# Kernel tuning notes

Measured on AMD Instinct MI355X. Metric: run time of the kernel, lower is better.

The kernel has to match this reference:

```python
import jax, jax.numpy as jnp
import numpy as np

DIM, NH, NKV, HD = 4096, 32, 8, 128
N_REP = NH // NKV
START_POS = 32767  # decode position; cache holds positions [0, START_POS)


def _rope(x, cos, sin):
    # x: (B, L, H, D); cos/sin: (L, D/2). Complex multiply on (even, odd) pairs.
    b, l, h, d = x.shape
    xr = x.reshape(b, l, h, d // 2, 2)
    x0, x1 = xr[..., 0], xr[..., 1]
    c = cos[None, :, None, :]
    s = sin[None, :, None, :]
    o0 = x0 * c - x1 * s
    o1 = x0 * s + x1 * c
    return jnp.stack([o0, o1], axis=-1).reshape(b, l, h, d)


def setup_inputs() -> dict:
    key = jax.random.key(0)
    ks = jax.random.split(key, 8)
    x = jax.random.normal(ks[0], (1, 1, DIM), jnp.float32)
    # real RoPE angles for the current position
    inv_freq = 1.0 / (10000.0 ** (np.arange(0, HD, 2, dtype=np.float32) / HD))
    ang = jnp.asarray((START_POS * inv_freq)[None, :], jnp.float32)  # (1, 64)
    freqs_cos = jnp.cos(ang)
    freqs_sin = jnp.sin(ang)
    k_cache = jax.random.normal(ks[1], (START_POS, NKV, HD), jnp.float32)
    v_cache = jax.random.normal(ks[2], (START_POS, NKV, HD), jnp.float32)
    sd = 1.0 / np.sqrt(DIM)
    wq = jax.random.normal(ks[3], (NH * HD, DIM), jnp.float32) * sd
    wk = jax.random.normal(ks[4], (NKV * HD, DIM), jnp.float32) * sd
    wv = jax.random.normal(ks[5], (NKV * HD, DIM), jnp.float32) * sd
    wo = jax.random.normal(ks[6], (DIM, NH * HD), jnp.float32) * sd
    return {"x": x, "freqs_cos": freqs_cos, "freqs_sin": freqs_sin,
            "k_cache": k_cache, "v_cache": v_cache,
            "wq": wq, "wk": wk, "wv": wv, "wo": wo,
            "start_pos": START_POS}


def reference(x, freqs_cos, freqs_sin, k_cache, v_cache, wq, wk, wv, wo, start_pos):
    bsz, seqlen, _ = x.shape  # (1, 1, DIM)
    q = (x @ wq.T).reshape(bsz, seqlen, NH, HD)
    k = (x @ wk.T).reshape(bsz, seqlen, NKV, HD)
    v = (x @ wv.T).reshape(bsz, seqlen, NKV, HD)
    q = _rope(q, freqs_cos, freqs_sin)
    k = _rope(k, freqs_cos, freqs_sin)
    # push current token KV and fetch full history (offloader fetch over all
    # blocks 0..start_pos//BLOCK == plain concat of cache + current token)
    k_full = jnp.concatenate([k_cache, k[0]], axis=0)  # (T, NKV, HD), T = start_pos+1
    v_full = jnp.concatenate([v_cache, v[0]], axis=0)
    # GQA repeat_kv: (T, NKV, HD) -> (1, NH, T, HD)
    T = k_full.shape[0]
    k_h = jnp.repeat(k_full, N_REP, axis=1).transpose(1, 0, 2)[None]  # (1, NH, T, HD)
    v_h = jnp.repeat(v_full, N_REP, axis=1).transpose(1, 0, 2)[None]
    qh = q.transpose(0, 2, 1, 3)  # (1, NH, 1, HD)
    scores = jnp.einsum("bhqd,bhtd->bhqt", qh, k_h) / jnp.sqrt(jnp.float32(HD))
    probs = jax.nn.softmax(scores, axis=-1)
    out = jnp.einsum("bhqt,bhtd->bhqd", probs, v_h)  # (1, NH, 1, HD)
    out = out.transpose(0, 2, 1, 3).reshape(bsz, seqlen, NH * HD)
    return out @ wo.T
```

## Files before the change

kernel.cpp:

```cpp
#include <hip/hip_runtime.h>
#include <math.h>


#define DIM 4096
#define NH 32
#define NKV 8
#define HD 128
#define NREP 4
#define RSPLIT 128

typedef float f32x4 __attribute__((ext_vector_type(4)));

__global__ __launch_bounds__(256) void qkv_rope_kernel(
    const float* __restrict__ x, const float* __restrict__ fc,
    const float* __restrict__ fs, const float* __restrict__ wq,
    const float* __restrict__ wk, const float* __restrict__ wv,
    float* __restrict__ q_rope, float* __restrict__ k_new,
    float* __restrict__ v_new) {
  int wave = blockIdx.x * 4 + (threadIdx.x >> 6);
  int lane = threadIdx.x & 63;
  const float* W;
  float* dst;
  int r0;
  bool rope;
  if (wave < 2048) {
    W = wq; dst = q_rope; r0 = wave * 2; rope = true;
  } else if (wave < 2560) {
    W = wk; dst = k_new; r0 = (wave - 2048) * 2; rope = true;
  } else {
    W = wv; dst = v_new; r0 = (wave - 2560) * 2; rope = false;
  }
  const float4* x4 = (const float4*)x;
  const float4* w0 = (const float4*)(W + (size_t)r0 * DIM);
  const float4* w1 = (const float4*)(W + (size_t)(r0 + 1) * DIM);
  float a0 = 0.f, a1 = 0.f;
#pragma unroll 4
  for (int c = lane; c < DIM / 4; c += 64) {
    float4 xv = x4[c];
    float4 u = w0[c];
    float4 v = w1[c];
    a0 += xv.x * u.x + xv.y * u.y + xv.z * u.z + xv.w * u.w;
    a1 += xv.x * v.x + xv.y * v.y + xv.z * v.z + xv.w * v.w;
  }
  for (int off = 32; off > 0; off >>= 1) {
    a0 += __shfl_down(a0, off, 64);
    a1 += __shfl_down(a1, off, 64);
  }
  if (lane == 0) {
    if (rope) {
      int j = (r0 & (HD - 1)) >> 1;
      float c = fc[j], s = fs[j];
      dst[r0]     = a0 * c - a1 * s;
      dst[r0 + 1] = a0 * s + a1 * c;
    } else {
      dst[r0]     = a0;
      dst[r0 + 1] = a1;
    }
  }
}

#define LD4(p) (*(const float4*)(p))
#define NT4(p) (__builtin_nontemporal_load((const f32x4*)(p)))

#define DOT4(sv, h)                                                         \
  sv = A.x * qf[h][0] + A.y * qf[h][1] + A.z * qf[h][2] + A.w * qf[h][3] +  \
       B.x * qf[h][4] + B.y * qf[h][5] + B.z * qf[h][6] + B.w * qf[h][7];

#define PV8(h, e)                                                           \
  acc[h][0] += (e)*VA.x; acc[h][1] += (e)*VA.y;                             \
  acc[h][2] += (e)*VA.z; acc[h][3] += (e)*VA.w;                             \
  acc[h][4] += (e)*VB.x; acc[h][5] += (e)*VB.y;                             \
  acc[h][6] += (e)*VB.z; acc[h][7] += (e)*VB.w;

#define STEP(KA_, KB_, VA_, VB_, VALID)                                     \
  {                                                                         \
    auto A = KA_; auto B = KB_;                                             \
    float s0, s1, s2, s3;                                                   \
    DOT4(s0, 0); DOT4(s1, 1); DOT4(s2, 2); DOT4(s3, 3);                     \
    float pp = hi8 ? s2 : s0, pq = hi8 ? s0 : s2;                           \
    pp += __shfl_xor(pq, 8, 64);                                            \
    float rr = hi8 ? s3 : s1, rs = hi8 ? s1 : s3;                           \
    rr += __shfl_xor(rs, 8, 64);                                            \
    float u = hi4 ? rr : pp, uvx = hi4 ? pp : rr;                           \
    u += __shfl_xor(uvx, 4, 64);                                            \
    u += __shfl_xor(u, 1, 64);                                              \
    u += __shfl_xor(u, 2, 64);                                              \
    float u4 = __shfl_xor(u, 4, 64);                                        \
    float u8 = __shfl_xor(u, 8, 64);                                        \
    float u12 = __shfl_xor(u4, 8, 64);                                      \
    float q0 = hi4 ? u4 : u,   q1 = hi4 ? u : u4;                           \
    float q2 = hi4 ? u12 : u8, q3 = hi4 ? u8 : u12;                         \
    float w0 = hi8 ? q2 : q0, w1 = hi8 ? q3 : q1;                           \
    float w2 = hi8 ? q0 : q2, w3 = hi8 ? q1 : q3;                           \
    float e0 = __expf((VALID) ? w0 * scale : -1e30f);                       \
    float e1 = __expf((VALID) ? w1 * scale : -1e30f);                       \
    float e2 = __expf((VALID) ? w2 * scale : -1e30f);                       \
    float e3 = __expf((VALID) ? w3 * scale : -1e30f);                       \
    lsum[0] += e0; lsum[1] += e1; lsum[2] += e2; lsum[3] += e3;             \
    auto VA = VA_; auto VB = VB_;                                           \
    PV8(0, e0) PV8(1, e1) PV8(2, e2) PV8(3, e3)                             \
  }

__global__ __launch_bounds__(256, 4) void attn_partial_kernel(
    const float* __restrict__ q_rope, const float* __restrict__ k_cache,
    const float* __restrict__ v_cache, const float* __restrict__ k_new,
    const float* __restrict__ v_new, float* __restrict__ partial_m,
    float* __restrict__ partial_l, float* __restrict__ partial_o,
    int start_pos, int T, int CH) {
  int g = blockIdx.x % NKV;
  int split = blockIdx.x / NKV;
  int t0 = split * CH;
  int tid = threadIdx.x;
  int wvi = tid >> 6;
  int lane = tid & 63;
  int grp = lane >> 4;
  int lig = lane & 15;
  int tl0 = wvi * 4 + grp;
  int dbase = lig * 8;
  bool hi8 = (lig & 8) != 0, hi4 = (lig & 4) != 0;

  __shared__ float s_wacc[4][4][HD];
  __shared__ float s_wl[4][4];

  float qf[4][8];
#pragma unroll
  for (int h = 0; h < 4; ++h)
#pragma unroll
    for (int e = 0; e < 8; ++e)
      qf[h][e] = q_rope[(g * NREP + h) * HD + dbase + e];

  float lsum[4] = {0.f, 0.f, 0.f, 0.f};
  float acc[4][8];
#pragma unroll
  for (int h = 0; h < 4; ++h)
#pragma unroll
    for (int e = 0; e < 8; ++e) acc[h][e] = 0.f;

  const float scale = 0.08838834764831845f;
  int iters = CH >> 4;
  bool full = (t0 + CH + 16 <= start_pos);
  const size_t kstep = (size_t)16 * NKV * HD;

  if (full) {
    const float* kp = k_cache + ((size_t)(t0 + tl0) * NKV + g) * HD + dbase;
    const float* vp = v_cache + ((size_t)(t0 + tl0) * NKV + g) * HD + dbase;
    f32x4 KA0 = NT4(kp), KB0 = NT4(kp + 4);
    f32x4 VA0 = NT4(vp), VB0 = NT4(vp + 4);
    kp += kstep; vp += kstep;
    for (int i = 0; i < iters; i += 2) {
      f32x4 KA1 = NT4(kp), KB1 = NT4(kp + 4);
      f32x4 VA1 = NT4(vp), VB1 = NT4(vp + 4);
      kp += kstep; vp += kstep;
      __builtin_amdgcn_sched_barrier(0);
      STEP(KA0, KB0, VA0, VB0, true);
      KA0 = NT4(kp); KB0 = NT4(kp + 4);
      VA0 = NT4(vp); VB0 = NT4(vp + 4);
      kp += kstep; vp += kstep;
      __builtin_amdgcn_sched_barrier(0);
      STEP(KA1, KB1, VA1, VB1, true);
    }
  } else {
    for (int i = 0; i < iters; ++i) {
      int t = t0 + i * 16 + tl0;
      bool valid = (t < T);
      const float* kp;
      const float* vp;
      if (t < start_pos) {
        kp = k_cache + ((size_t)t * NKV + g) * HD;
        vp = v_cache + ((size_t)t * NKV + g) * HD;
      } else {
        kp = k_new + (size_t)g * HD;
        vp = v_new + (size_t)g * HD;
      }
      f32x4 KA = NT4(kp + dbase), KB = NT4(kp + dbase + 4);
      f32x4 VAx = NT4(vp + dbase), VBx = NT4(vp + dbase + 4);
      STEP(KA, KB, VAx, VBx, valid);
    }
  }

#pragma unroll
  for (int h = 0; h < 4; ++h) {
    float lh = lsum[h];
    lh += __shfl_xor(lh, 16, 64);
    lh += __shfl_xor(lh, 32, 64);
    lsum[h] = lh;
#pragma unroll
    for (int e = 0; e < 8; ++e) {
      float a = acc[h][e];
      a += __shfl_xor(a, 16, 64);
      a += __shfl_xor(a, 32, 64);
      acc[h][e] = a;
    }
  }
  if (grp == 0) {
#pragma unroll
    for (int h = 0; h < 4; ++h)
#pragma unroll
      for (int e = 0; e < 8; ++e) s_wacc[wvi][h][dbase + e] = acc[h][e];
    if (lig == 0) {
#pragma unroll
      for (int h = 0; h < 4; ++h) s_wl[wvi][h] = lsum[h];
    }
  }
  __syncthreads();
  for (int o = tid; o < NREP * HD; o += 256) {
    int h = o >> 7, d = o & (HD - 1);
    float sum = s_wacc[0][h][d] + s_wacc[1][h][d] + s_wacc[2][h][d] +
                s_wacc[3][h][d];
    partial_o[((size_t)(g * NREP + h) * RSPLIT + split) * HD + d] = sum;
  }
  if (tid < NREP) {
    int hg = g * NREP + tid;
    partial_m[hg * RSPLIT + split] = 0.f;
    partial_l[hg * RSPLIT + split] =
        s_wl[0][tid] + s_wl[1][tid] + s_wl[2][tid] + s_wl[3][tid];
  }
}

__global__ __launch_bounds__(256) void combine_kernel(
    const float* __restrict__ partial_m, const float* __restrict__ partial_l,
    const float* __restrict__ partial_o, float* __restrict__ attn_out) {
  int h = blockIdx.x;
  int tid = threadIdx.x;
  __shared__ float s_m[RSPLIT], s_l[RSPLIT];
  __shared__ float s_acc[2][HD];
  if (tid < RSPLIT) {
    s_m[tid] = partial_m[h * RSPLIT + tid];
    s_l[tid] = partial_l[h * RSPLIT + tid];
  }
  __syncthreads();
  float M = -1e30f;
  for (int s = 0; s < RSPLIT; ++s) M = fmaxf(M, s_m[s]);
  float L = 0.f;
  for (int s = 0; s < RSPLIT; ++s) L += s_l[s] * __expf(s_m[s] - M);
  int d = tid & (HD - 1), half = tid >> 7;
  int hn = RSPLIT >> 1;
  float acc = 0.f;
#pragma unroll 4
  for (int s = half * hn; s < half * hn + hn; ++s)
    acc += __expf(s_m[s] - M) * partial_o[((size_t)h * RSPLIT + s) * HD + d];
  s_acc[half][d] = acc;
  __syncthreads();
  if (half == 0) attn_out[h * HD + d] = (s_acc[0][d] + s_acc[1][d]) / L;
}

__global__ __launch_bounds__(256) void out_gemv_kernel(
    const float* __restrict__ attn, const float* __restrict__ wo,
    float* __restrict__ out) {
  int row = blockIdx.x * 4 + (threadIdx.x >> 6);
  int lane = threadIdx.x & 63;
  const float4* a4 = (const float4*)attn;
  const float4* w4 = (const float4*)(wo + (size_t)row * DIM);
  float a = 0.f;
#pragma unroll 4
  for (int c = lane; c < DIM / 4; c += 64) {
    float4 av = a4[c];
    float4 wv = w4[c];
    a += av.x * wv.x + av.y * wv.y + av.z * wv.z + av.w * wv.w;
  }
  for (int off = 32; off > 0; off >>= 1) a += __shfl_down(a, off, 64);
  if (lane == 0) out[row] = a;
}

extern "C" void kernel_launch(void* const* d_in, const int* in_sizes, int n_in,
                              void* d_out, int out_size, void* d_ws,
                              size_t ws_size, hipStream_t stream) {
  const float* x       = (const float*)d_in[0];
  const float* fc      = (const float*)d_in[1];
  const float* fs      = (const float*)d_in[2];
  const float* k_cache = (const float*)d_in[3];
  const float* v_cache = (const float*)d_in[4];
  const float* wq      = (const float*)d_in[5];
  const float* wk      = (const float*)d_in[6];
  const float* wv      = (const float*)d_in[7];
  const float* wo      = (const float*)d_in[8];
  float* out = (float*)d_out;

  int start_pos = in_sizes[3] / (NKV * HD);
  int T = start_pos + 1;
  int CH = ((T + RSPLIT - 1) / RSPLIT + 15) & ~15;

  float* ws = (float*)d_ws;
  float* q_rope    = ws;
  float* k_new     = ws + 4096;
  float* v_new     = ws + 5120;
  float* attn_out  = ws + 6144;
  float* partial_m = ws + 10240;
  float* partial_l = partial_m + NH * RSPLIT;
  float* partial_o = partial_l + NH * RSPLIT;

  qkv_rope_kernel<<<768, 256, 0, stream>>>(x, fc, fs, wq, wk, wv, q_rope,
                                           k_new, v_new);
  attn_partial_kernel<<<NKV * RSPLIT, 256, 0, stream>>>(
      q_rope, k_cache, v_cache, k_new, v_new, partial_m, partial_l, partial_o,
      start_pos, T, CH);
  combine_kernel<<<NH, 256, 0, stream>>>(partial_m, partial_l, partial_o,
                                         attn_out);
  out_gemv_kernel<<<1024, 256, 0, stream>>>(attn_out, wo, out);
}
```

Baseline: 92.83 us.

## Replace split-KV combine kernel with atomic accumulation and fold normalization into output GEMV

Partial attention outputs and softmax denominators are now accumulated with atomicAdd into a single buffer, which the QKV kernel zeroes first. This removes the separate combine kernel launch and the partial buffer round trip. The 1/L normalization moves into the output projection GEMV. In exchange, the partial kernel's tail sees atomic contention (128 splits per element), and the float summation order becomes nondeterministic. It relies on the fixed max of zero already used before, so no max rescaling is needed.

```diff
diff --git a/kernel.cpp b/kernel.cpp
--- a/kernel.cpp
+++ b/kernel.cpp
@@ -1,6 +1,5 @@
 #include <hip/hip_runtime.h>
 #include <math.h>
-
 
 #define DIM 4096
 #define NH 32
@@ -16,7 +15,10 @@
     const float* __restrict__ fs, const float* __restrict__ wq,
     const float* __restrict__ wk, const float* __restrict__ wv,
     float* __restrict__ q_rope, float* __restrict__ k_new,
-    float* __restrict__ v_new) {
+    float* __restrict__ v_new, float* __restrict__ attn_raw) {
+  if (blockIdx.x == 0) {
+    for (int i = threadIdx.x; i < NH * HD + NH; i += 256) attn_raw[i] = 0.f;
+  }
   int wave = blockIdx.x * 4 + (threadIdx.x >> 6);
   int lane = threadIdx.x & 63;
   const float* W;
@@ -104,9 +106,8 @@
 __global__ __launch_bounds__(256, 4) void attn_partial_kernel(
     const float* __restrict__ q_rope, const float* __restrict__ k_cache,
     const float* __restrict__ v_cache, const float* __restrict__ k_new,
-    const float* __restrict__ v_new, float* __restrict__ partial_m,
-    float* __restrict__ partial_l, float* __restrict__ partial_o,
-    int start_pos, int T, int CH) {
+    const float* __restrict__ v_new, float* __restrict__ attn_raw,
+    float* __restrict__ L_raw, int start_pos, int T, int CH) {
   int g = blockIdx.x % NKV;
   int split = blockIdx.x / NKV;
   int t0 = split * CH;
@@ -207,56 +208,31 @@
     int h = o >> 7, d = o & (HD - 1);
     float sum = s_wacc[0][h][d] + s_wacc[1][h][d] + s_wacc[2][h][d] +
                 s_wacc[3][h][d];
-    partial_o[((size_t)(g * NREP + h) * RSPLIT + split) * HD + d] = sum;
+    atomicAdd(&attn_raw[(g * NREP + h) * HD + d], sum);
   }
   if (tid < NREP) {
-    int hg = g * NREP + tid;
-    partial_m[hg * RSPLIT + split] = 0.f;
-    partial_l[hg * RSPLIT + split] =
-        s_wl[0][tid] + s_wl[1][tid] + s_wl[2][tid] + s_wl[3][tid];
-  }
-}
-
-__global__ __launch_bounds__(256) void combine_kernel(
-    const float* __restrict__ partial_m, const float* __restrict__ partial_l,
-    const float* __restrict__ partial_o, float* __restrict__ attn_out) {
-  int h = blockIdx.x;
-  int tid = threadIdx.x;
-  __shared__ float s_m[RSPLIT], s_l[RSPLIT];
-  __shared__ float s_acc[2][HD];
-  if (tid < RSPLIT) {
-    s_m[tid] = partial_m[h * RSPLIT + tid];
-    s_l[tid] = partial_l[h * RSPLIT + tid];
-  }
+    atomicAdd(&L_raw[g * NREP + tid],
+              s_wl[0][tid] + s_wl[1][tid] + s_wl[2][tid] + s_wl[3][tid]);
+  }
+}
+
+__global__ __launch_bounds__(256) void out_gemv_kernel(
+    const float* __restrict__ attn_raw, const float* __restrict__ L_raw,
+    const float* __restrict__ wo, float* __restrict__ out) {
+  __shared__ float s_invL[NH];
+  if (threadIdx.x < NH) s_invL[threadIdx.x] = 1.f / L_raw[threadIdx.x];
   __syncthreads();
-  float M = -1e30f;
-  for (int s = 0; s < RSPLIT; ++s) M = fmaxf(M, s_m[s]);
-  float L = 0.f;
-  for (int s = 0; s < RSPLIT; ++s) L += s_l[s] * __expf(s_m[s] - M);
-  int d = tid & (HD - 1), half = tid >> 7;
-  int hn = RSPLIT >> 1;
-  float acc = 0.f;
-#pragma unroll 4
-  for (int s = half * hn; s < half * hn + hn; ++s)
-    acc += __expf(s_m[s] - M) * partial_o[((size_t)h * RSPLIT + s) * HD + d];
-  s_acc[half][d] = acc;
-  __syncthreads();
-  if (half == 0) attn_out[h * HD + d] = (s_acc[0][d] + s_acc[1][d]) / L;
-}
-
-__global__ __launch_bounds__(256) void out_gemv_kernel(
-    const float* __restrict__ attn, const float* __restrict__ wo,
-    float* __restrict__ out) {
   int row = blockIdx.x * 4 + (threadIdx.x >> 6);
   int lane = threadIdx.x & 63;
-  const float4* a4 = (const float4*)attn;
+  const float4* a4 = (const float4*)attn_raw;
   const float4* w4 = (const float4*)(wo + (size_t)row * DIM);
   float a = 0.f;
 #pragma unroll 4
   for (int c = lane; c < DIM / 4; c += 64) {
     float4 av = a4[c];
     float4 wv = w4[c];
-    a += av.x * wv.x + av.y * wv.y + av.z * wv.z + av.w * wv.w;
+    float il = s_invL[c >> 5];
+    a += (av.x * wv.x + av.y * wv.y + av.z * wv.z + av.w * wv.w) * il;
   }
   for (int off = 32; off > 0; off >>= 1) a += __shfl_down(a, off, 64);
   if (lane == 0) out[row] = a;
@@ -281,20 +257,16 @@
   int CH = ((T + RSPLIT - 1) / RSPLIT + 15) & ~15;
 
   float* ws = (float*)d_ws;
-  float* q_rope    = ws;
-  float* k_new     = ws + 4096;
-  float* v_new     = ws + 5120;
-  float* attn_out  = ws + 6144;
-  float* partial_m = ws + 10240;
-  float* partial_l = partial_m + NH * RSPLIT;
-  float* partial_o = partial_l + NH * RSPLIT;
+  float* q_rope   = ws;
+  float* k_new    = ws + 4096;
+  float* v_new    = ws + 5120;
+  float* attn_raw = ws + 6144;
+  float* L_raw    = attn_raw + NH * HD;
 
   qkv_rope_kernel<<<768, 256, 0, stream>>>(x, fc, fs, wq, wk, wv, q_rope,
-                                           k_new, v_new);
+                                           k_new, v_new, attn_raw);
   attn_partial_kernel<<<NKV * RSPLIT, 256, 0, stream>>>(
-      q_rope, k_cache, v_cache, k_new, v_new, partial_m, partial_l, partial_o,
+      q_rope, k_cache, v_cache, k_new, v_new, attn_raw, L_raw,
       start_pos, T, CH);
-  combine_kernel<<<NH, 256, 0, stream>>>(partial_m, partial_l, partial_o,
-                                         attn_out);
-  out_gemv_kernel<<<1024, 256, 0, stream>>>(attn_out, wo, out);
-}
+  out_gemv_kernel<<<1024, 256, 0, stream>>>(attn_raw, L_raw, wo, out);
+}
```

After: 92.29 us. About the same (-0.6%).
